# Performance work log

Hardware: AMD Instinct MI355X
Metric: run time of the kernel (lower is better)

## Reference

```python
import jax, jax.numpy as jnp
import numpy as np

BS, NN, D = 16, 1024, 256      # graphs, nodes/graph, d_model
N = BS * NN                     # total nodes
DEG = 8                         # avg degree
HEADS = 2                       # sa_heads == pine_heads == 2
DK = 64                         # d_k == d_v
PH = 256                        # pine_hidden


def _gat(x, src, dst, W, asrc, adst, b, concat):
    # PyG GATConv: lin -> per-head alpha -> leaky_relu -> segment softmax over dst -> scatter-add
    H, C = asrc.shape
    h = (x @ W).reshape(-1, H, C)                       # [N,H,C]
    a = jnp.sum(h * asrc[None], -1)[src] + jnp.sum(h * adst[None], -1)[dst]  # [E,H]
    a = jax.nn.leaky_relu(a, 0.2)
    amax = jax.ops.segment_max(a, dst, num_segments=N)
    ex = jnp.exp(a - amax[dst])
    den = jax.ops.segment_sum(ex, dst, num_segments=N)
    w = ex / (den[dst] + 1e-16)                         # [E,H]
    out = jax.ops.segment_sum(h[src] * w[:, :, None], dst, num_segments=N)  # [N,H,C]
    out = out.reshape(N, H * C) if concat else out.mean(1)
    return out + b


def _forward(edge_index, q, k, v, Wq, Wk, Wv, Wfc,
             g1_W, g1_asrc, g1_adst, g1_b, lin1_W, lin1_b,
             g2_W, g2_asrc, g2_adst, g2_b, lin2_W, lin2_b,
             g3_W, g3_asrc, g3_adst, g3_b, lin3_W, lin3_b,
             ln_g, ln_b):
    loop = jnp.arange(N, dtype=edge_index.dtype)        # GATConv adds self-loops
    src = jnp.concatenate([edge_index[0], loop])
    dst = jnp.concatenate([edge_index[1], loop])
    x = q.reshape(N, D)
    x = jax.nn.elu(_gat(x, src, dst, g1_W, g1_asrc, g1_adst, g1_b, True) + x @ lin1_W + lin1_b)
    x = jax.nn.elu(_gat(x, src, dst, g2_W, g2_asrc, g2_adst, g2_b, True) + x @ lin2_W + lin2_b)
    x = _gat(x, src, dst, g3_W, g3_asrc, g3_adst, g3_b, False) + x @ lin3_W + lin3_b
    xg = x.reshape(BS, NN, HEADS * DK)                  # graph branch [bs,n,128]

    qh = (q @ Wq).reshape(BS, NN, HEADS, DK).transpose(0, 2, 1, 3)
    kh = (k @ Wk).reshape(BS, NN, HEADS, DK).transpose(0, 2, 1, 3)
    vh = (v @ Wv).reshape(BS, NN, HEADS, DK).transpose(0, 2, 1, 3)
    scale = 1.0 / jnp.sqrt(jnp.float32(DK))
    attn = jax.nn.softmax(jnp.einsum('bhqd,bhkd->bhqk', qh * scale, kh), axis=-1)
    o = jnp.einsum('bhqk,bhkd->bhqd', attn, vh).transpose(0, 2, 1, 3).reshape(BS, NN, HEADS * DK)

    cat = jnp.concatenate([xg, o], axis=-1)             # [bs,n,(2+2)*d_v]
    out = cat @ Wfc + q                                  # residual (dropout = identity in eval)
    mu = out.mean(-1, keepdims=True)
    var = jnp.mean((out - mu) ** 2, -1, keepdims=True)
    y = (out - mu) / jnp.sqrt(var + 1e-6) * ln_g + ln_b
    return y, attn


def setup_inputs():
    key = jax.random.key(0)
    ks = jax.random.split(key, 40)
    def rn(i, shape, s=0.05):
        return jax.random.normal(ks[i], shape, dtype=jnp.float32) * s
    q = jax.random.normal(ks[0], (BS, NN, D), dtype=jnp.float32)
    k = jax.random.normal(ks[1], (BS, NN, D), dtype=jnp.float32)
    v = jax.random.normal(ks[2], (BS, NN, D), dtype=jnp.float32)
    Eg = NN * DEG
    src = jax.random.randint(ks[3], (BS, Eg), 0, NN)
    dst = jax.random.randint(ks[4], (BS, Eg), 0, NN)
    off = (jnp.arange(BS) * NN)[:, None]
    edge_index = jnp.stack([(src + off).reshape(-1), (dst + off).reshape(-1)]).astype(jnp.int32)
    HD2 = HEADS * PH  # 512
    return {
        'q': q, 'k': k, 'v': v, 'edge_index': edge_index,
        'Wq': rn(5, (D, HEADS * DK)), 'Wk': rn(6, (D, HEADS * DK)), 'Wv': rn(7, (D, HEADS * DK)),
        'Wfc': rn(8, (2 * HEADS * DK, D)),
        'g1_W': rn(9, (D, HD2)), 'g1_asrc': rn(10, (HEADS, PH)), 'g1_adst': rn(11, (HEADS, PH)),
        'g1_b': jnp.zeros((HD2,), jnp.float32),
        'lin1_W': rn(12, (D, HD2)), 'lin1_b': jnp.zeros((HD2,), jnp.float32),
        'g2_W': rn(13, (HD2, HD2)), 'g2_asrc': rn(14, (HEADS, PH)), 'g2_adst': rn(15, (HEADS, PH)),
        'g2_b': jnp.zeros((HD2,), jnp.float32),
        'lin2_W': rn(16, (HD2, HD2)), 'lin2_b': jnp.zeros((HD2,), jnp.float32),
        'g3_W': rn(17, (HD2, HEADS * HEADS * DK)), 'g3_asrc': rn(18, (HEADS, HEADS * DK)),
        'g3_adst': rn(19, (HEADS, HEADS * DK)), 'g3_b': jnp.zeros((HEADS * DK,), jnp.float32),
        'lin3_W': rn(20, (HD2, HEADS * DK)), 'lin3_b': jnp.zeros((HEADS * DK,), jnp.float32),
        'ln_g': jnp.ones((D,), jnp.float32), 'ln_b': jnp.zeros((D,), jnp.float32),
    }


def reference(q, k, v, edge_index, Wq, Wk, Wv, Wfc,
              g1_W, g1_asrc, g1_adst, g1_b, lin1_W, lin1_b,
              g2_W, g2_asrc, g2_adst, g2_b, lin2_W, lin2_b,
              g3_W, g3_asrc, g3_adst, g3_b, lin3_W, lin3_b,
              ln_g, ln_b):
    return _forward(edge_index, q, k, v, Wq, Wk, Wv, Wfc,
                    g1_W, g1_asrc, g1_adst, g1_b, lin1_W, lin1_b,
                    g2_W, g2_asrc, g2_adst, g2_b, lin2_W, lin2_b,
                    g3_W, g3_asrc, g3_adst, g3_b, lin3_W, lin3_b,
                    ln_g, ln_b)
```

## Files before the change

### kernel.cpp

```cpp
#include <hip/hip_runtime.h>

#define BSZ 16
#define NNODE 1024
#define NT (BSZ*NNODE)
#define EG 131072
#define ET (EG+NT)

typedef unsigned short bfu;
typedef __attribute__((ext_vector_type(8))) short short8v;
typedef __attribute__((ext_vector_type(4))) float f32x4;

typedef __attribute__((address_space(1))) const unsigned gU32;
typedef __attribute__((address_space(3))) unsigned lU32;
#define GLL16(gp, lp) __builtin_amdgcn_global_load_lds((gU32*)(gp), (lU32*)(lp), 16, 0, 0)

__device__ __forceinline__ float b2f(unsigned u) { return __uint_as_float(u << 16); }
__device__ __forceinline__ bfu f2b(float f) {
  unsigned u = __float_as_uint(f);
  u += 0x7fffu + ((u >> 16) & 1u);
  return (bfu)(u >> 16);
}
__device__ __forceinline__ void unpack8(uint4 u, float* f) {
  f[0] = b2f(u.x & 0xffffu); f[1] = b2f(u.x >> 16);
  f[2] = b2f(u.y & 0xffffu); f[3] = b2f(u.y >> 16);
  f[4] = b2f(u.z & 0xffffu); f[5] = b2f(u.z >> 16);
  f[6] = b2f(u.w & 0xffffu); f[7] = b2f(u.w >> 16);
}
__device__ __forceinline__ void edge_sd(const int* __restrict__ ei, int e, int& s, int& d) {
  if (e < EG) { s = ei[e]; d = ei[EG + e]; } else { s = e - EG; d = e - EG; }
}
__device__ __forceinline__ int swz(int c) {
  int r = c >> 2;
  return (c & ~3) | ((c & 3) ^ ((r & 3) ^ ((r >> 2) & 3)));
}

template<int EPI>
__global__ __launch_bounds__(256)
void mgemm(const bfu* __restrict__ A, int lda, long long sA,
           const bfu* __restrict__ Bt, int ldb, long long sB,
           int K,
           bfu* __restrict__ outb, float* __restrict__ outf, int ldo, long long sO,
           const float* __restrict__ b1, const float* __restrict__ b2,
           const bfu* __restrict__ agg, int aggld,
           const float* __restrict__ resid,
           const float* __restrict__ asrc, const float* __restrict__ adst,
           float* __restrict__ av_s, float* __restrict__ av_d)
{
  __shared__ bfu As[128 * 32];
  __shared__ bfu Bs[128 * 32];
  const int tid = threadIdx.x;
  const int z = blockIdx.z;
  const int n0 = blockIdx.x * 128, r0 = blockIdx.y * 128;
  const bfu* Az = A + (size_t)z * sA;
  const bfu* Bz = Bt + (size_t)z * sB;

  const int w = tid >> 6, l = tid & 63;
  const int wr = w >> 1, wc = w & 1;
  const int lr = l & 15;
  const int k8 = l >> 4;

  f32x4 acc[4][4] = {};

  const int s0c = swz(tid), s1c = swz(tid + 256);
  const bfu* ga0 = Az + (size_t)(r0 + (s0c >> 2)) * lda + (s0c & 3) * 8;
  const bfu* ga1 = Az + (size_t)(r0 + (s1c >> 2)) * lda + (s1c & 3) * 8;
  const bfu* gb0 = Bz + (size_t)(n0 + (s0c >> 2)) * ldb + (s0c & 3) * 8;
  const bfu* gb1 = Bz + (size_t)(n0 + (s1c >> 2)) * ldb + (s1c & 3) * 8;
  bfu* la0 = As + tid * 8;
  bfu* la1 = As + (tid + 256) * 8;
  bfu* lb0 = Bs + tid * 8;
  bfu* lb1 = Bs + (tid + 256) * 8;

  for (int k0 = 0; k0 < K; k0 += 32) {
    __syncthreads();
    GLL16(ga0, la0); GLL16(ga1, la1);
    GLL16(gb0, lb0); GLL16(gb1, lb1);
    ga0 += 32; ga1 += 32; gb0 += 32; gb1 += 32;
    __syncthreads();
    short8v af[4], bfr[4];
    #pragma unroll
    for (int mi = 0; mi < 4; ++mi) {
      const int R = wr * 64 + mi * 16 + lr;
      af[mi] = *(const short8v*)(As + swz(R * 4 + k8) * 8);
    }
    #pragma unroll
    for (int ni = 0; ni < 4; ++ni) {
      const int R = wc * 64 + ni * 16 + lr;
      bfr[ni] = *(const short8v*)(Bs + swz(R * 4 + k8) * 8);
    }
    #pragma unroll
    for (int mi = 0; mi < 4; ++mi)
      #pragma unroll
      for (int ni = 0; ni < 4; ++ni)
        acc[mi][ni] = __builtin_amdgcn_mfma_f32_16x16x32_bf16(af[mi], bfr[ni], acc[mi][ni], 0, 0, 0);
  }

  const int rr = k8 * 4;
  float ps[4][4], pd[4][4];
  if (EPI == 0 || EPI == 7) {
    #pragma unroll
    for (int mi = 0; mi < 4; ++mi)
      #pragma unroll
      for (int i = 0; i < 4; ++i) { ps[mi][i] = 0.f; pd[mi][i] = 0.f; }
  }

  #pragma unroll
  for (int mi = 0; mi < 4; ++mi) {
    #pragma unroll
    for (int ni = 0; ni < 4; ++ni) {
      #pragma unroll
      for (int i = 0; i < 4; ++i) {
        const int r = r0 + wr * 64 + mi * 16 + rr + i;
        const int cc = n0 + wc * 64 + ni * 16 + lr;
        float val = acc[mi][ni][i];
        if (EPI == 0) {
          outb[(size_t)r * ldo + cc] = f2b(val);
          ps[mi][i] = fmaf(val, asrc[cc], ps[mi][i]);
          pd[mi][i] = fmaf(val, adst[cc], pd[mi][i]);
        } else if (EPI == 1) {
          val += b1[cc] + b2[cc] + b2f(agg[(size_t)r * aggld + cc]);
          val = val > 0.f ? val : expm1f(val);
          outb[(size_t)r * ldo + cc] = f2b(val);
        } else if (EPI == 2) {
          val += b1[cc] + b2[cc]
               + 0.5f * (b2f(agg[(size_t)r * aggld + cc]) + b2f(agg[(size_t)r * aggld + 128 + cc]));
          outb[(size_t)r * ldo + cc] = f2b(val);
        } else if (EPI == 3) {
          outf[(size_t)r * ldo + cc] = val + resid[(size_t)r * ldo + cc];
        } else if (EPI == 7) {
          float e = expf(val);
          outb[(size_t)z * sO + (size_t)r * ldo + cc] = f2b(e);
          ps[mi][i] += e;
        } else {
          if (z < 2) {
            outb[(size_t)z * 2097152 + ((size_t)((r >> 10) * 2 + (cc >> 6))) * 65536
                 + (size_t)(r & 1023) * 64 + (cc & 63)] = f2b(val);
          } else {
            outb[4194304 + ((size_t)((r >> 10) * 2 + (cc >> 6))) * 65536
                 + (size_t)(cc & 63) * 1024 + (r & 1023)] = f2b(val);
          }
        }
      }
    }
  }

  if (EPI == 0) {
    const int half = ldo >> 1;
    const int hd = n0 / half;
    const int blk = (n0 & (half - 1)) >> 7;
    #pragma unroll
    for (int mi = 0; mi < 4; ++mi) {
      #pragma unroll
      for (int i = 0; i < 4; ++i) {
        float s = ps[mi][i], d = pd[mi][i];
        #pragma unroll
        for (int m = 1; m < 16; m <<= 1) { s += __shfl_xor(s, m); d += __shfl_xor(d, m); }
        if (lr == 0) {
          const int r = r0 + wr * 64 + mi * 16 + rr + i;
          av_s[((size_t)r * 2 + hd) * 4 + blk * 2 + wc] = s;
          av_d[((size_t)r * 2 + hd) * 4 + blk * 2 + wc] = d;
        }
      }
    }
  } else if (EPI == 7) {
    #pragma unroll
    for (int mi = 0; mi < 4; ++mi) {
      #pragma unroll
      for (int i = 0; i < 4; ++i) {
        float s = ps[mi][i];
        #pragma unroll
        for (int m = 1; m < 16; m <<= 1) s += __shfl_xor(s, m);
        if (lr == 0) {
          const int r = r0 + wr * 64 + mi * 16 + rr + i;
          av_s[((size_t)z * 1024 + r) * 16 + ((n0 >> 7) << 1) + wc] = s;
        }
      }
    }
  }
}

__global__ __launch_bounds__(256)
void pv_k(const bfu* __restrict__ Pb, const bfu* __restrict__ vt,
          const float* __restrict__ rowsum16, bfu* __restrict__ catb)
{
  __shared__ bfu As[128 * 32];
  __shared__ bfu Bs[64 * 32];
  const int tid = threadIdx.x;
  const int bh = blockIdx.z;
  const int r0 = blockIdx.y * 128;
  const bfu* Az = Pb + (size_t)bh * 1048576;
  const bfu* Bz = vt + (size_t)bh * 65536;
  const int w = tid >> 6, l = tid & 63;
  const int lr = l & 15, k8 = l >> 4;

  f32x4 acc[2][4] = {};

  const int s0c = swz(tid), s1c = swz(tid + 256);
  const bfu* ga0 = Az + (size_t)(r0 + (s0c >> 2)) * 1024 + (s0c & 3) * 8;
  const bfu* ga1 = Az + (size_t)(r0 + (s1c >> 2)) * 1024 + (s1c & 3) * 8;
  const bfu* gb0 = Bz + (size_t)(s0c >> 2) * 1024 + (s0c & 3) * 8;
  bfu* la0 = As + tid * 8;
  bfu* la1 = As + (tid + 256) * 8;
  bfu* lb0 = Bs + tid * 8;

  for (int k0 = 0; k0 < 1024; k0 += 32) {
    __syncthreads();
    GLL16(ga0, la0); GLL16(ga1, la1); GLL16(gb0, lb0);
    ga0 += 32; ga1 += 32; gb0 += 32;
    __syncthreads();
    short8v af[2], bfr[4];
    #pragma unroll
    for (int mi = 0; mi < 2; ++mi) {
      const int R = w * 32 + mi * 16 + lr;
      af[mi] = *(const short8v*)(As + swz(R * 4 + k8) * 8);
    }
    #pragma unroll
    for (int ni = 0; ni < 4; ++ni) {
      const int R = ni * 16 + lr;
      bfr[ni] = *(const short8v*)(Bs + swz(R * 4 + k8) * 8);
    }
    #pragma unroll
    for (int mi = 0; mi < 2; ++mi)
      #pragma unroll
      for (int ni = 0; ni < 4; ++ni)
        acc[mi][ni] = __builtin_amdgcn_mfma_f32_16x16x32_bf16(af[mi], bfr[ni], acc[mi][ni], 0, 0, 0);
  }

  const int b = bh >> 1, h = bh & 1;
  const int rr = k8 * 4;
  #pragma unroll
  for (int mi = 0; mi < 2; ++mi) {
    #pragma unroll
    for (int i = 0; i < 4; ++i) {
      const int qn = r0 + w * 32 + mi * 16 + rr + i;
      float sm = 0.f;
      #pragma unroll
      for (int j = 0; j < 16; ++j) sm += rowsum16[((size_t)bh * 1024 + qn) * 16 + j];
      const float inv = 1.f / sm;
      #pragma unroll
      for (int ni = 0; ni < 4; ++ni) {
        const int d = ni * 16 + lr;
        catb[((size_t)(b * 1024 + qn)) * 256 + 128 + h * 64 + d] = f2b(acc[mi][ni][i] * inv);
      }
    }
  }
}

__global__ __launch_bounds__(256)
void normk(const bfu* __restrict__ Pb, const float* __restrict__ rowsum16, float* __restrict__ Pf)
{
  const int w = threadIdx.x >> 6, l = threadIdx.x & 63;
  const size_t R = (size_t)blockIdx.x * 4 + w;
  const bfu* brow = Pb + R * 1024;
  float* frow = Pf + R * 1024;
  float sm = 0.f;
  #pragma unroll
  for (int j = 0; j < 16; ++j) sm += rowsum16[R * 16 + j];
  const float inv = 1.f / sm;
  uint4 u0 = *(const uint4*)(brow + l * 16);
  uint4 u1 = *(const uint4*)(brow + l * 16 + 8);
  float v[16];
  unpack8(u0, v); unpack8(u1, v + 8);
  #pragma unroll
  for (int j = 0; j < 4; ++j) {
    float4 o;
    o.x = v[j*4+0]*inv; o.y = v[j*4+1]*inv; o.z = v[j*4+2]*inv; o.w = v[j*4+3]*inv;
    *(float4*)(frow + l * 16 + j * 4) = o;
  }
}

__global__ __launch_bounds__(256)
void aconv3_k(const float* __restrict__ q, const float* __restrict__ k, const float* __restrict__ v,
              bfu* __restrict__ qo, bfu* __restrict__ ko, bfu* __restrict__ vo, int n4)
{
  const int i = blockIdx.x * 256 + threadIdx.x;
  if (i >= n4) return;
  const float* src = blockIdx.y == 0 ? q : (blockIdx.y == 1 ? k : v);
  bfu* dst = blockIdx.y == 0 ? qo : (blockIdx.y == 1 ? ko : vo);
  float4 x = ((const float4*)src)[i];
  uint2 o;
  o.x = (unsigned)f2b(x.x) | ((unsigned)f2b(x.y) << 16);
  o.y = (unsigned)f2b(x.z) | ((unsigned)f2b(x.w) << 16);
  ((uint2*)dst)[i] = o;
}

__global__ __launch_bounds__(256)
void wconv_all(const float* __restrict__ Wq, const float* __restrict__ Wk, const float* __restrict__ Wv,
               const float* __restrict__ Wfc, const float* __restrict__ g1W, const float* __restrict__ l1W,
               const float* __restrict__ g2W, const float* __restrict__ l2W, const float* __restrict__ g3W,
               const float* __restrict__ l3W, bfu* __restrict__ out)
{
  const int idx = blockIdx.x * 256 + threadIdx.x;
  const float* src; int kb, N, base; float sc = 1.f;
  if (idx < 98304)        { int wi = idx >> 15; base = wi << 15; src = wi == 0 ? Wq : (wi == 1 ? Wk : Wv); kb = 8; N = 128; if (wi == 0) sc = 0.125f; }
  else if (idx < 163840)  { base = 98304;  src = Wfc; kb = 8; N = 256; }
  else if (idx < 294912)  { base = 163840; src = g1W; kb = 8; N = 512; }
  else if (idx < 425984)  { base = 294912; src = l1W; kb = 8; N = 512; }
  else if (idx < 688128)  { base = 425984; src = g2W; kb = 9; N = 512; }
  else if (idx < 950272)  { base = 688128; src = l2W; kb = 9; N = 512; }
  else if (idx < 1081344) { base = 950272; src = g3W; kb = 9; N = 256; }
  else if (idx < 1146880) { base = 1081344; src = l3W; kb = 9; N = 128; }
  else return;
  const int local = idx - base;
  const int n = local >> kb, k = local & ((1 << kb) - 1);
  out[idx] = f2b(src[(size_t)k * N + n] * sc);
}

__global__ void zero_i(int* p, int n) {
  int i = blockIdx.x * 256 + threadIdx.x;
  if (i < n) p[i] = 0;
}

__global__ void csr_count(const int* __restrict__ ei, int* __restrict__ deg) {
  int e = blockIdx.x * 256 + threadIdx.x;
  if (e >= ET) return;
  int s, d; edge_sd(ei, e, s, d);
  atomicAdd(&deg[d], 1);
}
__global__ __launch_bounds__(1024)
void csr_scan(const int* __restrict__ deg, int* __restrict__ rowptr, int* __restrict__ fillc) {
  __shared__ int sums[1024];
  const int t = threadIdx.x;
  const int base = t * 16;
  int loc[16]; int s = 0;
  #pragma unroll
  for (int k = 0; k < 16; ++k) { loc[k] = deg[base + k]; s += loc[k]; }
  sums[t] = s;
  __syncthreads();
  for (int off = 1; off < 1024; off <<= 1) {
    int v = (t >= off) ? sums[t - off] : 0;
    __syncthreads();
    sums[t] += v;
    __syncthreads();
  }
  int run = sums[t] - s;
  #pragma unroll
  for (int k = 0; k < 16; ++k) { rowptr[base + k] = run; fillc[base + k] = run; run += loc[k]; }
  if (t == 1023) rowptr[NT] = sums[1023];
}
__global__ void csr_fill(const int* __restrict__ ei, int* __restrict__ fillc, int* __restrict__ srcs) {
  int e = blockIdx.x * 256 + threadIdx.x;
  if (e >= ET) return;
  int s, d; edge_sd(ei, e, s, d);
  int pos = atomicAdd(&fillc[d], 1);
  srcs[pos] = s;
}

template<int CT, int NBLK>
__global__ __launch_bounds__(256)
void aggf_k(const int* __restrict__ rowptr, const int* __restrict__ srcs,
            const float* __restrict__ avsp, const float* __restrict__ avdp,
            const bfu* __restrict__ h, bfu* __restrict__ agg)
{
  const int n = blockIdx.x, tid = threadIdx.x;
  float ad0 = avdp[(size_t)n * 8 + 0] + avdp[(size_t)n * 8 + 1];
  float ad1 = avdp[(size_t)n * 8 + 4] + avdp[(size_t)n * 8 + 5];
  if (NBLK > 1) {
    ad0 += avdp[(size_t)n * 8 + 2] + avdp[(size_t)n * 8 + 3];
    ad1 += avdp[(size_t)n * 8 + 6] + avdp[(size_t)n * 8 + 7];
  }
  float a0 = 0.f, a1 = 0.f, sum0 = 0.f, sum1 = 0.f;
  const int beg = rowptr[n], end = rowptr[n + 1];
  for (int idx = beg; idx < end; ++idx) {
    const int s = srcs[idx];
    float as0 = avsp[(size_t)s * 8 + 0] + avsp[(size_t)s * 8 + 1];
    float as1 = avsp[(size_t)s * 8 + 4] + avsp[(size_t)s * 8 + 5];
    if (NBLK > 1) {
      as0 += avsp[(size_t)s * 8 + 2] + avsp[(size_t)s * 8 + 3];
      as1 += avsp[(size_t)s * 8 + 6] + avsp[(size_t)s * 8 + 7];
    }
    float al0 = as0 + ad0; al0 = al0 > 0.f ? al0 : 0.2f * al0;
    float al1 = as1 + ad1; al1 = al1 > 0.f ? al1 : 0.2f * al1;
    const float e0 = expf(al0), e1 = expf(al1);
    sum0 += e0; sum1 += e1;
    if (CT == 512) {
      a0 = fmaf(e0, b2f(h[(size_t)s * 512 + tid]), a0);
      a1 = fmaf(e1, b2f(h[(size_t)s * 512 + 256 + tid]), a1);
    } else {
      const float ev = tid < 128 ? e0 : e1;
      a0 = fmaf(ev, b2f(h[(size_t)s * 256 + tid]), a0);
    }
  }
  if (CT == 512) {
    agg[(size_t)n * 512 + tid] = f2b(a0 / (sum0 + 1e-16f));
    agg[(size_t)n * 512 + 256 + tid] = f2b(a1 / (sum1 + 1e-16f));
  } else {
    const float sv = tid < 128 ? sum0 : sum1;
    agg[(size_t)n * 256 + tid] = f2b(a0 / (sv + 1e-16f));
  }
}

__global__ __launch_bounds__(256)
void ln_k(const float* __restrict__ x, const float* __restrict__ g, const float* __restrict__ bta,
          float* __restrict__ y)
{
  const int r = blockIdx.x, tid = threadIdx.x;
  float v = x[(size_t)r * 256 + tid];
  float s = v;
  #pragma unroll
  for (int off = 32; off; off >>= 1) s += __shfl_xor(s, off);
  __shared__ float red[4], red2[4];
  const int w = tid >> 6, lane = tid & 63;
  if (lane == 0) red[w] = s;
  __syncthreads();
  float mu = (red[0] + red[1] + red[2] + red[3]) * (1.f / 256.f);
  float dv = v - mu;
  float q2 = dv * dv;
  #pragma unroll
  for (int off = 32; off; off >>= 1) q2 += __shfl_xor(q2, off);
  if (lane == 0) red2[w] = q2;
  __syncthreads();
  float var = (red2[0] + red2[1] + red2[2] + red2[3]) * (1.f / 256.f);
  y[(size_t)r * 256 + tid] = dv * rsqrtf(var + 1e-6f) * g[tid] + bta[tid];
}

extern "C" void kernel_launch(void* const* d_in, const int* in_sizes, int n_in,
                              void* d_out, int out_size, void* d_ws, size_t ws_size,
                              hipStream_t stream)
{
  const float* q   = (const float*)d_in[0];
  const float* kin = (const float*)d_in[1];
  const float* vin = (const float*)d_in[2];
  const int*   ei  = (const int*)d_in[3];
  const float* Wq  = (const float*)d_in[4];
  const float* Wk  = (const float*)d_in[5];
  const float* Wv  = (const float*)d_in[6];
  const float* Wfc = (const float*)d_in[7];
  const float* g1W = (const float*)d_in[8],  *g1as = (const float*)d_in[9],  *g1ad = (const float*)d_in[10];
  const float* l1W = (const float*)d_in[12], *l1b = (const float*)d_in[13], *g1b = (const float*)d_in[11];
  const float* g2W = (const float*)d_in[14], *g2as = (const float*)d_in[15], *g2ad = (const float*)d_in[16], *g2b = (const float*)d_in[17];
  const float* l2W = (const float*)d_in[18], *l2b = (const float*)d_in[19];
  const float* g3W = (const float*)d_in[20], *g3as = (const float*)d_in[21], *g3ad = (const float*)d_in[22], *g3b = (const float*)d_in[23];
  const float* l3W = (const float*)d_in[24], *l3b = (const float*)d_in[25];
  const float* lng = (const float*)d_in[26], *lnb = (const float*)d_in[27];

  float* ybuf = (float*)d_out;
  float* attn_out = ybuf + (size_t)NT * 256;
  bfu* catb = (bfu*)d_out;

  char* ap = (char*)attn_out;
  auto take_a = [&](size_t bytes) -> void* {
    void* r = (void*)ap; ap += (bytes + 255) & ~(size_t)255; return r;
  };
  bfu* q_bf = (bfu*)take_a((size_t)NT * 256 * 2);
  bfu* k_bf = (bfu*)take_a((size_t)NT * 256 * 2);
  bfu* v_bf = (bfu*)take_a((size_t)NT * 256 * 2);
  bfu* aggb  = (bfu*)take_a((size_t)NT * 512 * 2);
  float* avsp = (float*)take_a((size_t)NT * 8 * 4);
  float* avdp = (float*)take_a((size_t)NT * 8 * 4);
  int* deg    = (int*)take_a((size_t)NT * 4);
  int* rowptr = (int*)take_a((size_t)(NT + 1) * 4);
  int* fillc  = (int*)take_a((size_t)NT * 4);
  int* srcs   = (int*)take_a((size_t)ET * 4);

  char* p = (char*)d_ws;
  auto take = [&](size_t bytes) -> void* {
    void* r = (void*)p; p += (bytes + 255) & ~(size_t)255; return r;
  };
  bfu* hbuf = (bfu*)take((size_t)NT * 512 * 2);
  bfu* x1   = (bfu*)take((size_t)NT * 512 * 2);
  bfu* x2   = (bfu*)take((size_t)NT * 512 * 2);
  bfu* wall = (bfu*)take((size_t)1146880 * 2);
  bfu* Pbuf = (bfu*)take((size_t)32 * 1048576 * 2);
  float* rowsum16 = (float*)take((size_t)32 * 1024 * 16 * 4);

  bfu* WqT  = wall;
  bfu* WfcT = wall + 98304;
  bfu* g1Wt = wall + 163840;
  bfu* l1Wt = wall + 294912;
  bfu* g2Wt = wall + 425984;
  bfu* l2Wt = wall + 688128;
  bfu* g3Wt = wall + 950272;
  bfu* l3Wt = wall + 1081344;

  bfu* qh2  = hbuf;
  bfu* khb2 = hbuf + (size_t)2 * 1024 * 1024;
  bfu* vt   = hbuf + (size_t)4 * 1024 * 1024;
  float* prelng = (float*)x1;

  const int EB = (ET + 255) / 256;
  const long long zs = 0;
  #define NOAL nullptr, nullptr, nullptr, nullptr

  aconv3_k<<<dim3(4096, 3), 256, 0, stream>>>(q, kin, vin, q_bf, k_bf, v_bf, NT * 64);
  wconv_all<<<4480, 256, 0, stream>>>(Wq, Wk, Wv, Wfc, g1W, l1W, g2W, l2W, g3W, l3W, wall);

  zero_i<<<(NT + 255) / 256, 256, 0, stream>>>(deg, NT);
  csr_count<<<EB, 256, 0, stream>>>(ei, deg);
  csr_scan<<<1, 1024, 0, stream>>>(deg, rowptr, fillc);
  csr_fill<<<EB, 256, 0, stream>>>(ei, fillc, srcs);

  mgemm<0><<<dim3(4, 128), 256, 0, stream>>>(q_bf, 256, zs, g1Wt, 256, zs, 256, hbuf, nullptr, 512, zs, nullptr, nullptr, nullptr, 0, nullptr, g1as, g1ad, avsp, avdp);
  aggf_k<512, 2><<<NT, 256, 0, stream>>>(rowptr, srcs, avsp, avdp, hbuf, aggb);
  mgemm<1><<<dim3(4, 128), 256, 0, stream>>>(q_bf, 256, zs, l1Wt, 256, zs, 256, x1, nullptr, 512, zs, l1b, g1b, aggb, 512, nullptr, NOAL);

  mgemm<0><<<dim3(4, 128), 256, 0, stream>>>(x1, 512, zs, g2Wt, 512, zs, 512, hbuf, nullptr, 512, zs, nullptr, nullptr, nullptr, 0, nullptr, g2as, g2ad, avsp, avdp);
  aggf_k<512, 2><<<NT, 256, 0, stream>>>(rowptr, srcs, avsp, avdp, hbuf, aggb);
  mgemm<1><<<dim3(4, 128), 256, 0, stream>>>(x1, 512, zs, l2Wt, 512, zs, 512, x2, nullptr, 512, zs, l2b, g2b, aggb, 512, nullptr, NOAL);

  mgemm<0><<<dim3(2, 128), 256, 0, stream>>>(x2, 512, zs, g3Wt, 512, zs, 512, hbuf, nullptr, 256, zs, nullptr, nullptr, nullptr, 0, nullptr, g3as, g3ad, avsp, avdp);
  aggf_k<256, 1><<<NT, 256, 0, stream>>>(rowptr, srcs, avsp, avdp, hbuf, aggb);
  mgemm<2><<<dim3(1, 128), 256, 0, stream>>>(x2, 512, zs, l3Wt, 512, zs, 512, catb, nullptr, 256, zs, l3b, g3b, aggb, 256, nullptr, NOAL);

  mgemm<8><<<dim3(1, 128, 3), 256, 0, stream>>>(q_bf, 256, (long long)NT * 256, WqT, 256, 32768LL, 256, qh2, nullptr, 0, zs, nullptr, nullptr, nullptr, 0, nullptr, NOAL);

  mgemm<7><<<dim3(8, 8, 32), 256, 0, stream>>>(qh2, 64, 65536LL, khb2, 64, 65536LL, 64, Pbuf, nullptr, 1024, 1048576LL, nullptr, nullptr, nullptr, 0, nullptr, nullptr, nullptr, rowsum16, nullptr);
  normk<<<8192, 256, 0, stream>>>(Pbuf, rowsum16, attn_out);
  pv_k<<<dim3(1, 8, 32), 256, 0, stream>>>(Pbuf, vt, rowsum16, catb);

  mgemm<3><<<dim3(2, 128), 256, 0, stream>>>(catb, 256, zs, WfcT, 256, zs, 256, nullptr, prelng, 256, zs, nullptr, nullptr, nullptr, 0, q, NOAL);
  ln_k<<<NT, 256, 0, stream>>>(prelng, lng, lnb, ybuf);
}
```

Before: 489.2 us.

## Double-buffer LDS tiles in GEMM kernels and fuse conversion launches

The mgemm and pv_k main loops now use two LDS buffers per operand. The next K-tile is loaded asynchronously into the idle buffer while MFMAs run on the current one, so each iteration needs one barrier instead of two. The separate input and weight bf16 conversion kernels are merged into a single launch using blockIdx.y to choose the work. This doubles LDS use per block, which may reduce occupancy.

Measured after the change: 505.4 us. 1.03x slower.

```diff
diff --git a/kernel.cpp b/kernel.cpp
--- a/kernel.cpp
+++ b/kernel.cpp
@@ -46,8 +46,8 @@
            const float* __restrict__ asrc, const float* __restrict__ adst,
            float* __restrict__ av_s, float* __restrict__ av_d)
 {
-  __shared__ bfu As[128 * 32];
-  __shared__ bfu Bs[128 * 32];
+  __shared__ bfu As[2][128 * 32];
+  __shared__ bfu Bs[2][128 * 32];
   const int tid = threadIdx.x;
   const int z = blockIdx.z;
   const int n0 = blockIdx.x * 128, r0 = blockIdx.y * 128;
@@ -66,33 +66,40 @@
   const bfu* ga1 = Az + (size_t)(r0 + (s1c >> 2)) * lda + (s1c & 3) * 8;
   const bfu* gb0 = Bz + (size_t)(n0 + (s0c >> 2)) * ldb + (s0c & 3) * 8;
   const bfu* gb1 = Bz + (size_t)(n0 + (s1c >> 2)) * ldb + (s1c & 3) * 8;
-  bfu* la0 = As + tid * 8;
-  bfu* la1 = As + (tid + 256) * 8;
-  bfu* lb0 = Bs + tid * 8;
-  bfu* lb1 = Bs + (tid + 256) * 8;
-
+
+  GLL16(ga0, As[0] + tid * 8);
+  GLL16(ga1, As[0] + (tid + 256) * 8);
+  GLL16(gb0, Bs[0] + tid * 8);
+  GLL16(gb1, Bs[0] + (tid + 256) * 8);
+  ga0 += 32; ga1 += 32; gb0 += 32; gb1 += 32;
+
+  int cur = 0;
   for (int k0 = 0; k0 < K; k0 += 32) {
     __syncthreads();
-    GLL16(ga0, la0); GLL16(ga1, la1);
-    GLL16(gb0, lb0); GLL16(gb1, lb1);
-    ga0 += 32; ga1 += 32; gb0 += 32; gb1 += 32;
-    __syncthreads();
+    if (k0 + 32 < K) {
+      GLL16(ga0, As[cur ^ 1] + tid * 8);
+      GLL16(ga1, As[cur ^ 1] + (tid + 256) * 8);
+      GLL16(gb0, Bs[cur ^ 1] + tid * 8);
+      GLL16(gb1, Bs[cur ^ 1] + (tid + 256) * 8);
+      ga0 += 32; ga1 += 32; gb0 += 32; gb1 += 32;
+    }
     short8v af[4], bfr[4];
     #pragma unroll
     for (int mi = 0; mi < 4; ++mi) {
       const int R = wr * 64 + mi * 16 + lr;
-      af[mi] = *(const short8v*)(As + swz(R * 4 + k8) * 8);
+      af[mi] = *(const short8v*)(As[cur] + swz(R * 4 + k8) * 8);
     }
     #pragma unroll
     for (int ni = 0; ni < 4; ++ni) {
       const int R = wc * 64 + ni * 16 + lr;
-      bfr[ni] = *(const short8v*)(Bs + swz(R * 4 + k8) * 8);
+      bfr[ni] = *(const short8v*)(Bs[cur] + swz(R * 4 + k8) * 8);
     }
     #pragma unroll
     for (int mi = 0; mi < 4; ++mi)
       #pragma unroll
       for (int ni = 0; ni < 4; ++ni)
         acc[mi][ni] = __builtin_amdgcn_mfma_f32_16x16x32_bf16(af[mi], bfr[ni], acc[mi][ni], 0, 0, 0);
+    cur ^= 1;
   }
 
   const int rr = k8 * 4;
@@ -183,8 +190,8 @@
 void pv_k(const bfu* __restrict__ Pb, const bfu* __restrict__ vt,
           const float* __restrict__ rowsum16, bfu* __restrict__ catb)
 {
-  __shared__ bfu As[128 * 32];
-  __shared__ bfu Bs[64 * 32];
+  __shared__ bfu As[2][128 * 32];
+  __shared__ bfu Bs[2][64 * 32];
   const int tid = threadIdx.x;
   const int bh = blockIdx.z;
   const int r0 = blockIdx.y * 128;
@@ -199,31 +206,38 @@
   const bfu* ga0 = Az + (size_t)(r0 + (s0c >> 2)) * 1024 + (s0c & 3) * 8;
   const bfu* ga1 = Az + (size_t)(r0 + (s1c >> 2)) * 1024 + (s1c & 3) * 8;
   const bfu* gb0 = Bz + (size_t)(s0c >> 2) * 1024 + (s0c & 3) * 8;
-  bfu* la0 = As + tid * 8;
-  bfu* la1 = As + (tid + 256) * 8;
-  bfu* lb0 = Bs + tid * 8;
-
+
+  GLL16(ga0, As[0] + tid * 8);
+  GLL16(ga1, As[0] + (tid + 256) * 8);
+  GLL16(gb0, Bs[0] + tid * 8);
+  ga0 += 32; ga1 += 32; gb0 += 32;
+
+  int cur = 0;
   for (int k0 = 0; k0 < 1024; k0 += 32) {
     __syncthreads();
-    GLL16(ga0, la0); GLL16(ga1, la1); GLL16(gb0, lb0);
-    ga0 += 32; ga1 += 32; gb0 += 32;
-    __syncthreads();
+    if (k0 + 32 < 1024) {
+      GLL16(ga0, As[cur ^ 1] + tid * 8);
+      GLL16(ga1, As[cur ^ 1] + (tid + 256) * 8);
+      GLL16(gb0, Bs[cur ^ 1] + tid * 8);
+      ga0 += 32; ga1 += 32; gb0 += 32;
+    }
     short8v af[2], bfr[4];
     #pragma unroll
     for (int mi = 0; mi < 2; ++mi) {
       const int R = w * 32 + mi * 16 + lr;
-      af[mi] = *(const short8v*)(As + swz(R * 4 + k8) * 8);
+      af[mi] = *(const short8v*)(As[cur] + swz(R * 4 + k8) * 8);
     }
     #pragma unroll
     for (int ni = 0; ni < 4; ++ni) {
       const int R = ni * 16 + lr;
-      bfr[ni] = *(const short8v*)(Bs + swz(R * 4 + k8) * 8);
+      bfr[ni] = *(const short8v*)(Bs[cur] + swz(R * 4 + k8) * 8);
     }
     #pragma unroll
     for (int mi = 0; mi < 2; ++mi)
       #pragma unroll
       for (int ni = 0; ni < 4; ++ni)
         acc[mi][ni] = __builtin_amdgcn_mfma_f32_16x16x32_bf16(af[mi], bfr[ni], acc[mi][ni], 0, 0, 0);
+    cur ^= 1;
   }
 
   const int b = bh >> 1, h = bh & 1;
@@ -270,26 +284,26 @@
 }
 
 __global__ __launch_bounds__(256)
-void aconv3_k(const float* __restrict__ q, const float* __restrict__ k, const float* __restrict__ v,
-              bfu* __restrict__ qo, bfu* __restrict__ ko, bfu* __restrict__ vo, int n4)
-{
-  const int i = blockIdx.x * 256 + threadIdx.x;
-  if (i >= n4) return;
-  const float* src = blockIdx.y == 0 ? q : (blockIdx.y == 1 ? k : v);
-  bfu* dst = blockIdx.y == 0 ? qo : (blockIdx.y == 1 ? ko : vo);
-  float4 x = ((const float4*)src)[i];
-  uint2 o;
-  o.x = (unsigned)f2b(x.x) | ((unsigned)f2b(x.y) << 16);
-  o.y = (unsigned)f2b(x.z) | ((unsigned)f2b(x.w) << 16);
-  ((uint2*)dst)[i] = o;
-}
-
-__global__ __launch_bounds__(256)
-void wconv_all(const float* __restrict__ Wq, const float* __restrict__ Wk, const float* __restrict__ Wv,
-               const float* __restrict__ Wfc, const float* __restrict__ g1W, const float* __restrict__ l1W,
-               const float* __restrict__ g2W, const float* __restrict__ l2W, const float* __restrict__ g3W,
-               const float* __restrict__ l3W, bfu* __restrict__ out)
-{
+void conv_all(const float* __restrict__ q, const float* __restrict__ k, const float* __restrict__ v,
+              bfu* __restrict__ qo, bfu* __restrict__ ko, bfu* __restrict__ vo,
+              const float* __restrict__ Wq, const float* __restrict__ Wk, const float* __restrict__ Wv,
+              const float* __restrict__ Wfc, const float* __restrict__ g1W, const float* __restrict__ l1W,
+              const float* __restrict__ g2W, const float* __restrict__ l2W, const float* __restrict__ g3W,
+              const float* __restrict__ l3W, bfu* __restrict__ out)
+{
+  const int zz = blockIdx.y;
+  if (zz < 3) {
+    const int i = blockIdx.x * 256 + threadIdx.x;
+    if (i >= NT * 64) return;
+    const float* src = zz == 0 ? q : (zz == 1 ? k : v);
+    bfu* dst = zz == 0 ? qo : (zz == 1 ? ko : vo);
+    float4 x = ((const float4*)src)[i];
+    uint2 o;
+    o.x = (unsigned)f2b(x.x) | ((unsigned)f2b(x.y) << 16);
+    o.y = (unsigned)f2b(x.z) | ((unsigned)f2b(x.w) << 16);
+    ((uint2*)dst)[i] = o;
+    return;
+  }
   const int idx = blockIdx.x * 256 + threadIdx.x;
   const float* src; int kb, N, base; float sc = 1.f;
   if (idx < 98304)        { int wi = idx >> 15; base = wi << 15; src = wi == 0 ? Wq : (wi == 1 ? Wk : Wv); kb = 8; N = 128; if (wi == 0) sc = 0.125f; }
@@ -302,8 +316,8 @@
   else if (idx < 1146880) { base = 1081344; src = l3W; kb = 9; N = 128; }
   else return;
   const int local = idx - base;
-  const int n = local >> kb, k = local & ((1 << kb) - 1);
-  out[idx] = f2b(src[(size_t)k * N + n] * sc);
+  const int n = local >> kb, kk = local & ((1 << kb) - 1);
+  out[idx] = f2b(src[(size_t)kk * N + n] * sc);
 }
 
 __global__ void zero_i(int* p, int n) {
@@ -482,8 +496,8 @@
   const long long zs = 0;
   #define NOAL nullptr, nullptr, nullptr, nullptr
 
-  aconv3_k<<<dim3(4096, 3), 256, 0, stream>>>(q, kin, vin, q_bf, k_bf, v_bf, NT * 64);
-  wconv_all<<<4480, 256, 0, stream>>>(Wq, Wk, Wv, Wfc, g1W, l1W, g2W, l2W, g3W, l3W, wall);
+  conv_all<<<dim3(4480, 4), 256, 0, stream>>>(q, kin, vin, q_bf, k_bf, v_bf,
+                                              Wq, Wk, Wv, Wfc, g1W, l1W, g2W, l2W, g3W, l3W, wall);
 
   zero_i<<<(NT + 255) / 256, 256, 0, stream>>>(deg, NT);
   csr_count<<<EB, 256, 0, stream>>>(ei, deg);
```

## Fuse attention normalization into PV kernel and merge conversion kernels

Applied to the files above, without the earlier changes.

The attention-probability normalization and fp32 write-out now happen inside the PV matmul kernel, reusing the bf16 P tile already staged in LDS. This removes the separate normalization pass that re-read the bf16 probability buffer. The input and weight bf16 conversion kernels are also merged into one launch. The risk is that the large fp32 attention write now comes from only a few hundred blocks, interleaved with the MFMA loop, which may limit achieved write bandwidth.

After: 478.6 us. 1.02x faster.

```diff
diff --git a/kernel.cpp b/kernel.cpp
--- a/kernel.cpp
+++ b/kernel.cpp
@@ -181,7 +181,8 @@
 
 __global__ __launch_bounds__(256)
 void pv_k(const bfu* __restrict__ Pb, const bfu* __restrict__ vt,
-          const float* __restrict__ rowsum16, bfu* __restrict__ catb)
+          const float* __restrict__ rowsum16, bfu* __restrict__ catb,
+          float* __restrict__ attn)
 {
   __shared__ bfu As[128 * 32];
   __shared__ bfu Bs[64 * 32];
@@ -196,18 +197,46 @@
   f32x4 acc[2][4] = {};
 
   const int s0c = swz(tid), s1c = swz(tid + 256);
-  const bfu* ga0 = Az + (size_t)(r0 + (s0c >> 2)) * 1024 + (s0c & 3) * 8;
-  const bfu* ga1 = Az + (size_t)(r0 + (s1c >> 2)) * 1024 + (s1c & 3) * 8;
+  const int rA0 = r0 + (s0c >> 2), rA1 = r0 + (s1c >> 2);
+  const bfu* ga0 = Az + (size_t)rA0 * 1024 + (s0c & 3) * 8;
+  const bfu* ga1 = Az + (size_t)rA1 * 1024 + (s1c & 3) * 8;
   const bfu* gb0 = Bz + (size_t)(s0c >> 2) * 1024 + (s0c & 3) * 8;
   bfu* la0 = As + tid * 8;
   bfu* la1 = As + (tid + 256) * 8;
   bfu* lb0 = Bs + tid * 8;
+
+  float sm0 = 0.f, sm1 = 0.f;
+  #pragma unroll
+  for (int j = 0; j < 16; ++j) {
+    sm0 += rowsum16[((size_t)bh * 1024 + rA0) * 16 + j];
+    sm1 += rowsum16[((size_t)bh * 1024 + rA1) * 16 + j];
+  }
+  const float invA0 = 1.f / sm0, invA1 = 1.f / sm1;
+  float* aout0 = attn + ((size_t)bh * 1024 + rA0) * 1024 + (s0c & 3) * 8;
+  float* aout1 = attn + ((size_t)bh * 1024 + rA1) * 1024 + (s1c & 3) * 8;
 
   for (int k0 = 0; k0 < 1024; k0 += 32) {
     __syncthreads();
     GLL16(ga0, la0); GLL16(ga1, la1); GLL16(gb0, lb0);
     ga0 += 32; ga1 += 32; gb0 += 32;
     __syncthreads();
+
+    {
+      uint4 u0 = *(const uint4*)la0;
+      uint4 u1 = *(const uint4*)la1;
+      float f0[8], f1[8];
+      unpack8(u0, f0); unpack8(u1, f1);
+      float4 o;
+      o.x = f0[0]*invA0; o.y = f0[1]*invA0; o.z = f0[2]*invA0; o.w = f0[3]*invA0;
+      *(float4*)(aout0 + k0) = o;
+      o.x = f0[4]*invA0; o.y = f0[5]*invA0; o.z = f0[6]*invA0; o.w = f0[7]*invA0;
+      *(float4*)(aout0 + k0 + 4) = o;
+      o.x = f1[0]*invA1; o.y = f1[1]*invA1; o.z = f1[2]*invA1; o.w = f1[3]*invA1;
+      *(float4*)(aout1 + k0) = o;
+      o.x = f1[4]*invA1; o.y = f1[5]*invA1; o.z = f1[6]*invA1; o.w = f1[7]*invA1;
+      *(float4*)(aout1 + k0 + 4) = o;
+    }
+
     short8v af[2], bfr[4];
     #pragma unroll
     for (int mi = 0; mi < 2; ++mi) {
@@ -247,49 +276,26 @@
 }
 
 __global__ __launch_bounds__(256)
-void normk(const bfu* __restrict__ Pb, const float* __restrict__ rowsum16, float* __restrict__ Pf)
+void conv_all(const float* __restrict__ q, const float* __restrict__ k, const float* __restrict__ v,
+              bfu* __restrict__ qo, bfu* __restrict__ ko, bfu* __restrict__ vo,
+              const float* __restrict__ Wq, const float* __restrict__ Wk, const float* __restrict__ Wv,
+              const float* __restrict__ Wfc, const float* __restrict__ g1W, const float* __restrict__ l1W,
+              const float* __restrict__ g2W, const float* __restrict__ l2W, const float* __restrict__ g3W,
+              const float* __restrict__ l3W, bfu* __restrict__ out)
 {
-  const int w = threadIdx.x >> 6, l = threadIdx.x & 63;
-  const size_t R = (size_t)blockIdx.x * 4 + w;
-  const bfu* brow = Pb + R * 1024;
-  float* frow = Pf + R * 1024;
-  float sm = 0.f;
-  #pragma unroll
-  for (int j = 0; j < 16; ++j) sm += rowsum16[R * 16 + j];
-  const float inv = 1.f / sm;
-  uint4 u0 = *(const uint4*)(brow + l * 16);
-  uint4 u1 = *(const uint4*)(brow + l * 16 + 8);
-  float v[16];
-  unpack8(u0, v); unpack8(u1, v + 8);
-  #pragma unroll
-  for (int j = 0; j < 4; ++j) {
-    float4 o;
-    o.x = v[j*4+0]*inv; o.y = v[j*4+1]*inv; o.z = v[j*4+2]*inv; o.w = v[j*4+3]*inv;
-    *(float4*)(frow + l * 16 + j * 4) = o;
-  }
-}
-
-__global__ __launch_bounds__(256)
-void aconv3_k(const float* __restrict__ q, const float* __restrict__ k, const float* __restrict__ v,
-              bfu* __restrict__ qo, bfu* __restrict__ ko, bfu* __restrict__ vo, int n4)
-{
-  const int i = blockIdx.x * 256 + threadIdx.x;
-  if (i >= n4) return;
-  const float* src = blockIdx.y == 0 ? q : (blockIdx.y == 1 ? k : v);
-  bfu* dst = blockIdx.y == 0 ? qo : (blockIdx.y == 1 ? ko : vo);
-  float4 x = ((const float4*)src)[i];
-  uint2 o;
-  o.x = (unsigned)f2b(x.x) | ((unsigned)f2b(x.y) << 16);
-  o.y = (unsigned)f2b(x.z) | ((unsigned)f2b(x.w) << 16);
-  ((uint2*)dst)[i] = o;
-}
-
-__global__ __launch_bounds__(256)
-void wconv_all(const float* __restrict__ Wq, const float* __restrict__ Wk, const float* __restrict__ Wv,
-               const float* __restrict__ Wfc, const float* __restrict__ g1W, const float* __restrict__ l1W,
-               const float* __restrict__ g2W, const float* __restrict__ l2W, const float* __restrict__ g3W,
-               const float* __restrict__ l3W, bfu* __restrict__ out)
-{
+  const int zz = blockIdx.y;
+  if (zz < 3) {
+    const int i = blockIdx.x * 256 + threadIdx.x;
+    if (i >= NT * 64) return;
+    const float* src = zz == 0 ? q : (zz == 1 ? k : v);
+    bfu* dst = zz == 0 ? qo : (zz == 1 ? ko : vo);
+    float4 x = ((const float4*)src)[i];
+    uint2 o;
+    o.x = (unsigned)f2b(x.x) | ((unsigned)f2b(x.y) << 16);
+    o.y = (unsigned)f2b(x.z) | ((unsigned)f2b(x.w) << 16);
+    ((uint2*)dst)[i] = o;
+    return;
+  }
   const int idx = blockIdx.x * 256 + threadIdx.x;
   const float* src; int kb, N, base; float sc = 1.f;
   if (idx < 98304)        { int wi = idx >> 15; base = wi << 15; src = wi == 0 ? Wq : (wi == 1 ? Wk : Wv); kb = 8; N = 128; if (wi == 0) sc = 0.125f; }
@@ -302,8 +308,8 @@
   else if (idx < 1146880) { base = 1081344; src = l3W; kb = 9; N = 128; }
   else return;
   const int local = idx - base;
-  const int n = local >> kb, k = local & ((1 << kb) - 1);
-  out[idx] = f2b(src[(size_t)k * N + n] * sc);
+  const int n = local >> kb, kk = local & ((1 << kb) - 1);
+  out[idx] = f2b(src[(size_t)kk * N + n] * sc);
 }
 
 __global__ void zero_i(int* p, int n) {
@@ -482,8 +488,8 @@
   const long long zs = 0;
   #define NOAL nullptr, nullptr, nullptr, nullptr
 
-  aconv3_k<<<dim3(4096, 3), 256, 0, stream>>>(q, kin, vin, q_bf, k_bf, v_bf, NT * 64);
-  wconv_all<<<4480, 256, 0, stream>>>(Wq, Wk, Wv, Wfc, g1W, l1W, g2W, l2W, g3W, l3W, wall);
+  conv_all<<<dim3(4480, 4), 256, 0, stream>>>(q, kin, vin, q_bf, k_bf, v_bf,
+                                              Wq, Wk, Wv, Wfc, g1W, l1W, g2W, l2W, g3W, l3W, wall);
 
   zero_i<<<(NT + 255) / 256, 256, 0, stream>>>(deg, NT);
   csr_count<<<EB, 256, 0, stream>>>(ei, deg);
@@ -505,8 +511,7 @@
   mgemm<8><<<dim3(1, 128, 3), 256, 0, stream>>>(q_bf, 256, (long long)NT * 256, WqT, 256, 32768LL, 256, qh2, nullptr, 0, zs, nullptr, nullptr, nullptr, 0, nullptr, NOAL);
 
   mgemm<7><<<dim3(8, 8, 32), 256, 0, stream>>>(qh2, 64, 65536LL, khb2, 64, 65536LL, 64, Pbuf, nullptr, 1024, 1048576LL, nullptr, nullptr, nullptr, 0, nullptr, nullptr, nullptr, rowsum16, nullptr);
-  normk<<<8192, 256, 0, stream>>>(Pbuf, rowsum16, attn_out);
-  pv_k<<<dim3(1, 8, 32), 256, 0, stream>>>(Pbuf, vt, rowsum16, catb);
+  pv_k<<<dim3(1, 8, 32), 256, 0, stream>>>(Pbuf, vt, rowsum16, catb, attn_out);
 
   mgemm<3><<<dim3(2, 128), 256, 0, stream>>>(catb, 256, zs, WfcT, 256, zs, 256, nullptr, prelng, 256, zs, nullptr, nullptr, nullptr, 0, q, NOAL);
   ln_k<<<NT, 256, 0, stream>>>(prelng, lng, lnb, ybuf);
```
